# Optimization experiments

Measured on AMD Instinct MI355X. Metric: run time of the kernel, lower is better.

The kernel has to match this reference:

```python
import jax, jax.numpy as jnp
import numpy as np


def dct_mat(N):
    # Orthonormal DCT-II matrix D, so dct(x, norm='ortho') along an axis = D @ x.
    n = jnp.arange(N, dtype=jnp.float32)
    k = jnp.arange(N, dtype=jnp.float32)[:, None]
    M = jnp.cos(jnp.pi * (n + 0.5) * k / N)  # [N, N]
    s = jnp.full((N, 1), jnp.sqrt(2.0 / N), dtype=jnp.float32).at[0, 0].set(jnp.sqrt(1.0 / N))
    return M * s


SCALE = 2


def setup_inputs() -> dict:
    key = jax.random.key(0)
    k1, _ = jax.random.split(key)
    x_lowres = jax.random.normal(k1, (16, 256, 64, 64), dtype=jnp.float32)
    sparse_mask = jnp.ones((1, 256, 1, 1), dtype=jnp.float32)
    return {"x_lowres": x_lowres, "sparse_mask": sparse_mask}


def reference(x_lowres, sparse_mask):
    B, C, H, W = x_lowres.shape
    H2, W2 = H * SCALE, W * SCALE

    DH, DW = dct_mat(H), dct_mat(W)
    # 2D ortho DCT: transform along W, then along H
    c = jnp.einsum('bchw,lw->bchl', x_lowres, DW)
    c = jnp.einsum('kh,bchl->bckl', DH, c)

    # Zero-pad high frequencies (bottom/right) up to target size
    c_pad = jnp.pad(c, ((0, 0), (0, 0), (0, H2 - H), (0, W2 - W)))

    # F.interpolate of a [1,C,1,1] map to (H2,W2) with bilinear/align_corners=False
    # is spatially constant per channel -> plain broadcast multiply is exact.
    c_mod = c_pad * sparse_mask

    # 2D ortho IDCT (DCT-III) at upsampled size: x = D^T @ y @ D
    DH2, DW2 = dct_mat(H2), dct_mat(W2)
    r = jnp.einsum('kn,bckl->bcnl', DH2, c_mod)
    out = jnp.einsum('bcnl,lm->bcnm', r, DW2)
    return out
```

## Files before the change

### kernel.cpp

```cpp
#include <hip/hip_runtime.h>


typedef __attribute__((ext_vector_type(8))) _Float16 f16x8;
typedef __attribute__((ext_vector_type(4))) _Float16 f16x4;
typedef __attribute__((ext_vector_type(4))) float f32x4;

#define NSLICES 4096
#define MFMA16(A, B, C) __builtin_amdgcn_mfma_f32_16x16x32_f16((A), (B), (C), 0, 0, 0)

__global__ void build_ut(_Float16* __restrict__ uf) {
    const int idx = blockIdx.x * 256 + threadIdx.x;
    const int n = idx >> 6;
    const int h = idx & 63;
    const float s0 = 0.125f;
    const float sk = 0.17677669529663687f;
    const float t0 = 0.088388347648318447f;
    const float tk = 0.125f;
    float acc = s0 * t0;
    #pragma unroll 4
    for (int k = 1; k < 64; ++k) {
        float a = cospif((float)((2 * h + 1) * k) * (1.0f / 128.0f));
        float b = cospif((float)((2 * n + 1) * k) * (1.0f / 256.0f));
        acc = fmaf(sk * tk * a, b, acc);
    }
    _Float16 hi = (_Float16)acc;
    _Float16 lo = (_Float16)(acc - (float)hi);
    const int j = n >> 4;
    const int lane = (n & 15) + 16 * ((h >> 3) & 3);
    const int kk = h >> 5;
    const int t = h & 7;
    const int base = ((j * 2 + kk) * 2) * 512 + lane * 8 + t;
    uf[base] = hi;
    uf[base + 512] = lo;
}

__global__ __launch_bounds__(256, 2)
void dct_fsr(const float* __restrict__ x, const float* __restrict__ mask,
             const _Float16* __restrict__ uf, float* __restrict__ out) {
    __shared__ _Float16 sRh[128 * 72];
    __shared__ _Float16 sRl[128 * 72];
    __shared__ float sOutW[4][16 * 132];

    const int tid = threadIdx.x;
    const int wid = tid >> 6;
    const int lane = tid & 63;
    const int l15 = lane & 15;
    const int lg = lane >> 4;
    const int slice = blockIdx.x;
    const float mval = mask[slice & 255];

    const f16x8* ufr = (const f16x8*)uf;

    const float* xp = x + (size_t)slice * 4096 + (16 * wid + l15) * 64 + 8 * lg;
    const float4 xa = *(const float4*)xp;
    const float4 xb = *(const float4*)(xp + 4);
    const float4 xc = *(const float4*)(xp + 32);
    const float4 xd = *(const float4*)(xp + 36);

    f16x8 ah0, al0, ah1, al1;
#define SPLIT(H, L, E, V)                      \
    {                                          \
        float y_ = (V) * mval;                 \
        _Float16 h_ = (_Float16)y_;            \
        H[E] = h_;                             \
        L[E] = (_Float16)(y_ - (float)h_);     \
    }
    SPLIT(ah0, al0, 0, xa.x) SPLIT(ah0, al0, 1, xa.y)
    SPLIT(ah0, al0, 2, xa.z) SPLIT(ah0, al0, 3, xa.w)
    SPLIT(ah0, al0, 4, xb.x) SPLIT(ah0, al0, 5, xb.y)
    SPLIT(ah0, al0, 6, xb.z) SPLIT(ah0, al0, 7, xb.w)
    SPLIT(ah1, al1, 0, xc.x) SPLIT(ah1, al1, 1, xc.y)
    SPLIT(ah1, al1, 2, xc.z) SPLIT(ah1, al1, 3, xc.w)
    SPLIT(ah1, al1, 4, xd.x) SPLIT(ah1, al1, 5, xd.y)
    SPLIT(ah1, al1, 6, xd.z) SPLIT(ah1, al1, 7, xd.w)
#undef SPLIT

    #pragma unroll
    for (int j = 0; j < 8; ++j) {
        const f16x8 bh0 = ufr[((j * 2 + 0) * 2 + 0) * 64 + lane];
        const f16x8 bl0 = ufr[((j * 2 + 0) * 2 + 1) * 64 + lane];
        const f16x8 bh1 = ufr[((j * 2 + 1) * 2 + 0) * 64 + lane];
        const f16x8 bl1 = ufr[((j * 2 + 1) * 2 + 1) * 64 + lane];
        f32x4 acc = {0.f, 0.f, 0.f, 0.f};
        acc = MFMA16(ah0, bh0, acc);
        acc = MFMA16(ah1, bh1, acc);
        acc = MFMA16(ah0, bl0, acc);
        acc = MFMA16(ah1, bl1, acc);
        acc = MFMA16(al0, bh0, acc);
        acc = MFMA16(al1, bh1, acc);
        const int m = 16 * j + l15;
        const int h0 = 16 * wid + 4 * lg;
        f16x4 rh, rl;
        #pragma unroll
        for (int r = 0; r < 4; ++r) {
            const float vv = acc[r];
            const _Float16 hi = (_Float16)vv;
            rh[r] = hi;
            rl[r] = (_Float16)(vv - (float)hi);
        }
        *(f16x4*)&sRh[m * 72 + h0] = rh;
        *(f16x4*)&sRl[m * 72 + h0] = rl;
    }
    __syncthreads();

    f16x8 Ah[2][2], Al[2][2];
    #pragma unroll
    for (int i = 0; i < 2; ++i) {
        const int ig = 2 * wid + i;
        #pragma unroll
        for (int kk = 0; kk < 2; ++kk) {
            Ah[i][kk] = ufr[((ig * 2 + kk) * 2 + 0) * 64 + lane];
            Al[i][kk] = ufr[((ig * 2 + kk) * 2 + 1) * 64 + lane];
        }
    }

    f32x4 acc2[2][8];
    #pragma unroll
    for (int i = 0; i < 2; ++i)
        #pragma unroll
        for (int j = 0; j < 8; ++j)
            acc2[i][j] = (f32x4){0.f, 0.f, 0.f, 0.f};

    #pragma unroll
    for (int j = 0; j < 8; ++j) {
        const int m = 16 * j + l15;
        const f16x8 bh0 = *(const f16x8*)&sRh[m * 72 + 0 + 8 * lg];
        const f16x8 bh1 = *(const f16x8*)&sRh[m * 72 + 32 + 8 * lg];
        const f16x8 bl0 = *(const f16x8*)&sRl[m * 72 + 0 + 8 * lg];
        const f16x8 bl1 = *(const f16x8*)&sRl[m * 72 + 32 + 8 * lg];
        #pragma unroll
        for (int i = 0; i < 2; ++i) {
            f32x4 a = acc2[i][j];
            a = MFMA16(Ah[i][0], bh0, a);
            a = MFMA16(Ah[i][1], bh1, a);
            a = MFMA16(Ah[i][0], bl0, a);
            a = MFMA16(Ah[i][1], bl1, a);
            a = MFMA16(Al[i][0], bh0, a);
            a = MFMA16(Al[i][1], bh1, a);
            acc2[i][j] = a;
        }
    }

    float* og = out + (size_t)slice * 16384;
    float* sw = sOutW[wid];
    #pragma unroll
    for (int i = 0; i < 2; ++i) {
        const int ig = 2 * wid + i;
        #pragma unroll
        for (int j = 0; j < 8; ++j) {
            const int mc = 16 * j + l15;
            #pragma unroll
            for (int r = 0; r < 4; ++r)
                sw[(4 * lg + r) * 132 + mc] = acc2[i][j][r];
        }
        #pragma unroll
        for (int it = 0; it < 8; ++it) {
            const int c = lane + 64 * it;
            const int row = c >> 5;
            const int m4 = (c & 31) * 4;
            const float4 v = *(const float4*)&sw[row * 132 + m4];
            *(float4*)&og[(size_t)(16 * ig + row) * 128 + m4] = v;
        }
    }
}

extern "C" void kernel_launch(void* const* d_in, const int* in_sizes, int n_in,
                              void* d_out, int out_size, void* d_ws, size_t ws_size,
                              hipStream_t stream) {
    const float* x = (const float*)d_in[0];
    const float* mask = (const float*)d_in[1];
    float* out = (float*)d_out;
    _Float16* uf = (_Float16*)d_ws;

    build_ut<<<32, 256, 0, stream>>>(uf);
    dct_fsr<<<NSLICES, 256, 0, stream>>>(x, mask, uf, out);
}
```

Measured before the change: 332.8 us.

## Drop LDS output staging and store MFMA results directly to raise occupancy

Removes the per-wave shared-memory transpose buffer for output and writes each MFMA accumulator element straight to global memory. The second-stage GEMM is restructured to process one row group at a time, which shrinks the live accumulator set. Launch bounds are raised from 2 to 4 blocks per CU. This cuts LDS usage and register pressure to allow more resident blocks. The cost is that global stores become scalar 4-byte writes (16 lanes contiguous per row) instead of coalesced float4 rows, which may reduce write efficiency.

```diff
diff --git a/kernel.cpp b/kernel.cpp
--- a/kernel.cpp
+++ b/kernel.cpp
@@ -34,12 +34,11 @@
     uf[base + 512] = lo;
 }
 
-__global__ __launch_bounds__(256, 2)
+__global__ __launch_bounds__(256, 4)
 void dct_fsr(const float* __restrict__ x, const float* __restrict__ mask,
              const _Float16* __restrict__ uf, float* __restrict__ out) {
     __shared__ _Float16 sRh[128 * 72];
     __shared__ _Float16 sRl[128 * 72];
-    __shared__ float sOutW[4][16 * 132];
 
     const int tid = threadIdx.x;
     const int wid = tid >> 6;
@@ -103,63 +102,32 @@
     }
     __syncthreads();
 
-    f16x8 Ah[2][2], Al[2][2];
+    float* og = out + (size_t)slice * 16384;
     #pragma unroll
     for (int i = 0; i < 2; ++i) {
         const int ig = 2 * wid + i;
-        #pragma unroll
-        for (int kk = 0; kk < 2; ++kk) {
-            Ah[i][kk] = ufr[((ig * 2 + kk) * 2 + 0) * 64 + lane];
-            Al[i][kk] = ufr[((ig * 2 + kk) * 2 + 1) * 64 + lane];
-        }
-    }
-
-    f32x4 acc2[2][8];
-    #pragma unroll
-    for (int i = 0; i < 2; ++i)
-        #pragma unroll
-        for (int j = 0; j < 8; ++j)
-            acc2[i][j] = (f32x4){0.f, 0.f, 0.f, 0.f};
-
-    #pragma unroll
-    for (int j = 0; j < 8; ++j) {
-        const int m = 16 * j + l15;
-        const f16x8 bh0 = *(const f16x8*)&sRh[m * 72 + 0 + 8 * lg];
-        const f16x8 bh1 = *(const f16x8*)&sRh[m * 72 + 32 + 8 * lg];
-        const f16x8 bl0 = *(const f16x8*)&sRl[m * 72 + 0 + 8 * lg];
-        const f16x8 bl1 = *(const f16x8*)&sRl[m * 72 + 32 + 8 * lg];
-        #pragma unroll
-        for (int i = 0; i < 2; ++i) {
-            f32x4 a = acc2[i][j];
-            a = MFMA16(Ah[i][0], bh0, a);
-            a = MFMA16(Ah[i][1], bh1, a);
-            a = MFMA16(Ah[i][0], bl0, a);
-            a = MFMA16(Ah[i][1], bl1, a);
-            a = MFMA16(Al[i][0], bh0, a);
-            a = MFMA16(Al[i][1], bh1, a);
-            acc2[i][j] = a;
-        }
-    }
-
-    float* og = out + (size_t)slice * 16384;
-    float* sw = sOutW[wid];
-    #pragma unroll
-    for (int i = 0; i < 2; ++i) {
-        const int ig = 2 * wid + i;
+        const f16x8 Ah0 = ufr[((ig * 2 + 0) * 2 + 0) * 64 + lane];
+        const f16x8 Al0 = ufr[((ig * 2 + 0) * 2 + 1) * 64 + lane];
+        const f16x8 Ah1 = ufr[((ig * 2 + 1) * 2 + 0) * 64 + lane];
+        const f16x8 Al1 = ufr[((ig * 2 + 1) * 2 + 1) * 64 + lane];
+        float* orow = og + (size_t)(16 * ig + 4 * lg) * 128 + l15;
         #pragma unroll
         for (int j = 0; j < 8; ++j) {
-            const int mc = 16 * j + l15;
+            const int m = 16 * j + l15;
+            const f16x8 bh0 = *(const f16x8*)&sRh[m * 72 + 0 + 8 * lg];
+            const f16x8 bh1 = *(const f16x8*)&sRh[m * 72 + 32 + 8 * lg];
+            const f16x8 bl0 = *(const f16x8*)&sRl[m * 72 + 0 + 8 * lg];
+            const f16x8 bl1 = *(const f16x8*)&sRl[m * 72 + 32 + 8 * lg];
+            f32x4 a = {0.f, 0.f, 0.f, 0.f};
+            a = MFMA16(Ah0, bh0, a);
+            a = MFMA16(Ah1, bh1, a);
+            a = MFMA16(Ah0, bl0, a);
+            a = MFMA16(Ah1, bl1, a);
+            a = MFMA16(Al0, bh0, a);
+            a = MFMA16(Al1, bh1, a);
             #pragma unroll
             for (int r = 0; r < 4; ++r)
-                sw[(4 * lg + r) * 132 + mc] = acc2[i][j][r];
-        }
-        #pragma unroll
-        for (int it = 0; it < 8; ++it) {
-            const int c = lane + 64 * it;
-            const int row = c >> 5;
-            const int m4 = (c & 31) * 4;
-            const float4 v = *(const float4*)&sw[row * 132 + m4];
-            *(float4*)&og[(size_t)(16 * ig + row) * 128 + m4] = v;
+                orow[(size_t)r * 128 + 16 * j] = a[r];
         }
     }
 }
```

Result: no change. 335.8 us (+0.9%).
